# Performance work log

Measured on AMD Instinct MI355X. Metric: run time of the kernel, lower is better.

The kernel has to match this reference:

```python
import jax, jax.numpy as jnp
import numpy as np

GS, GL, LS, LL, NA = 8, 8, 16, 8, 12
ALPHA = 0.5


def _rgb_to_lab(img):
    # img: (B,3,H,W) in [0,1]. Standard sRGB -> CIELab (kornia convention).
    lin = jnp.where(img > 0.04045, ((img + 0.055) / 1.055) ** 2.4, img / 12.92)
    r, g, b = lin[:, 0], lin[:, 1], lin[:, 2]
    x = 0.412453 * r + 0.357580 * g + 0.180423 * b
    y = 0.212671 * r + 0.715160 * g + 0.072169 * b
    z = 0.019334 * r + 0.119193 * g + 0.950227 * b
    xn, yn, zn = x / 0.950456, y, z / 1.088754
    f = lambda t: jnp.where(t > 0.008856, jnp.cbrt(t), 7.787 * t + 4.0 / 29.0)
    fx, fy, fz = f(xn), f(yn), f(zn)
    L = 116.0 * fy - 16.0
    a = 500.0 * (fx - fy)
    bb = 200.0 * (fy - fz)
    return L, a, bb


def _bilateral_slice(grid, img, guide):
    # grid: (B,12,s,s,l); img: (B,3,H,W); guide: (B,H,W) in [0,1]
    B, C, s, _, l = grid.shape
    _, _, H, W = img.shape
    g5 = jnp.transpose(grid, (0, 4, 2, 3, 1))  # (B, D=l, Hg=s, Wg=s, C)
    # align_corners=True coordinates, border padding == clamp
    fx = jnp.linspace(0.0, s - 1.0, W)                    # (W,)
    fy = jnp.linspace(0.0, s - 1.0, H)                    # (H,)
    fz = jnp.clip(guide * (l - 1.0), 0.0, l - 1.0)        # (B,H,W)
    x0 = jnp.floor(fx).astype(jnp.int32); x1 = jnp.minimum(x0 + 1, s - 1)
    y0 = jnp.floor(fy).astype(jnp.int32); y1 = jnp.minimum(y0 + 1, s - 1)
    z0 = jnp.floor(fz).astype(jnp.int32); z1 = jnp.minimum(z0 + 1, l - 1)
    wx = (fx - x0)[None, None, :, None]
    wy = (fy - y0)[None, :, None, None]
    wz = (fz - z0)[..., None]
    bi = jnp.arange(B)[:, None, None]
    yi0, yi1 = y0[None, :, None], y1[None, :, None]
    xi0, xi1 = x0[None, None, :], x1[None, None, :]

    def gat(zi, yi, xi):
        return g5[bi, zi, yi, xi]  # (B,H,W,C)

    def bilin(zi):
        c00 = gat(zi, yi0, xi0) * (1 - wx) + gat(zi, yi0, xi1) * wx
        c10 = gat(zi, yi1, xi0) * (1 - wx) + gat(zi, yi1, xi1) * wx
        return c00 * (1 - wy) + c10 * wy

    coeffs = bilin(z0) * (1 - wz) + bilin(z1) * wz       # (B,H,W,12)
    A = coeffs[..., :9].reshape(B, H, W, 3, 3)
    bvec = coeffs[..., 9:]
    img_hwc = jnp.transpose(img, (0, 2, 3, 1))           # (B,H,W,3)
    out = jnp.einsum('bhwck,bhwk->bhwc', A, img_hwc) + bvec
    return jnp.transpose(jnp.clip(out, 0.0, 1.0), (0, 3, 1, 2))


def setup_inputs() -> dict:
    key = jax.random.key(0)
    ks = jax.random.split(key, 16)
    B, H, W = 4, 896, 896
    n_h = n_w = 64
    inp = {
        'R_spatial': jax.random.normal(ks[0], (B, 256, n_h, n_w), jnp.float32),
        'F_sem': jax.random.normal(ks[1], (B, n_h * n_w, 384), jnp.float32),
        'img': jax.random.uniform(ks[2], (B, 3, H, W), jnp.float32),
        'n_h': n_h,
        'n_w': n_w,
    }
    sc = 0.02
    identity = np.array([1., 0., 0., 0., 1., 0., 0., 0., 1., 0., 0., 0.], np.float32)
    inp['dino_proj_w'] = jax.random.normal(ks[3], (128, 384), jnp.float32) * sc
    inp['dino_proj_b'] = jnp.zeros((128,), jnp.float32)
    inp['fusion_w'] = jax.random.normal(ks[4], (256, 384), jnp.float32) * sc
    inp['fusion_b'] = jnp.zeros((256,), jnp.float32)
    inp['g1_w'] = jax.random.normal(ks[5], (256, 256), jnp.float32) * sc
    inp['g1_b'] = jnp.zeros((256,), jnp.float32)
    inp['g2_w'] = jax.random.normal(ks[6], (NA * GS * GS * GL, 256), jnp.float32) * sc
    inp['g2_b'] = jnp.asarray(np.repeat(identity, GS * GS * GL))  # identity init
    inp['local_w'] = jax.random.normal(ks[7], (NA * LL, 256), jnp.float32) * sc
    inp['local_b'] = jnp.asarray(np.repeat(identity, LL))
    inp['guide_w1'] = jax.random.normal(ks[8], (64, 384), jnp.float32) * sc
    inp['guide_b1'] = jnp.zeros((64,), jnp.float32)
    inp['guide_w2'] = jax.random.normal(ks[9], (1, 64), jnp.float32) * sc
    inp['guide_b2'] = jnp.zeros((1,), jnp.float32)
    return inp


def reference(R_spatial, F_sem, img, n_h, n_w,
              dino_proj_w, dino_proj_b, fusion_w, fusion_b,
              g1_w, g1_b, g2_w, g2_b, local_w, local_b,
              guide_w1, guide_b1, guide_w2, guide_b2):
    B, _, H, W = img.shape
    # ---- GridNet ----
    F_sp = jnp.transpose(F_sem, (0, 2, 1)).reshape(B, 384, n_h, n_w)
    proj = jnp.einsum('bchw,oc->bohw', F_sp, dino_proj_w) + dino_proj_b[None, :, None, None]
    fused_in = jnp.concatenate([R_spatial, proj], axis=1)
    fused = jnp.einsum('bchw,oc->bohw', fused_in, fusion_w) + fusion_b[None, :, None, None]
    f_gap = fused.mean(axis=(-2, -1))                       # (B,256)
    h = jax.nn.relu(f_gap @ g1_w.T + g1_b)
    G_global = (h @ g2_w.T + g2_b).reshape(B, NA, GS, GS, GL)
    kh, kw = n_h // LS, n_w // LS
    pooled = fused.reshape(B, 256, LS, kh, LS, kw).mean(axis=(3, 5))
    lflat = jnp.einsum('bchw,oc->bohw', pooled, local_w) + local_b[None, :, None, None]
    G_local = jnp.transpose(lflat.reshape(B, NA, LL, LS, LS), (0, 1, 3, 4, 2))
    # ---- SemanticGuide ----
    L, a, bb = _rgb_to_lab(img)
    g_chroma = jnp.clip((0.5 * L + 0.25 * jnp.abs(a) + 0.25 * jnp.abs(bb)) / 114.0, 0.0, 1.0)
    hsem = jax.nn.relu(jnp.einsum('bnd,hd->bnh', F_sem, guide_w1) + guide_b1)
    g_sem_patch = jax.nn.sigmoid(jnp.einsum('bnh,oh->bno', hsem, guide_w2) + guide_b2)
    g_sem_patch = g_sem_patch.reshape(B, n_h, n_w, 1).transpose(0, 3, 1, 2)
    g_sem = jax.image.resize(g_sem_patch, (B, 1, H, W), 'bilinear')[:, 0]
    g = ALPHA * g_chroma + (1.0 - ALPHA) * g_sem
    # ---- slice + apply ----
    I_global = _bilateral_slice(G_global, img, g)
    I_local = _bilateral_slice(G_local, img, g)
    return I_global, I_local, G_global, G_local, g
```

## Files before the change

### kernel.cpp

```cpp
#include <hip/hip_runtime.h>
#include <math.h>

#define HWPIX 802816
#define OUT_IL 9633792
#define OUT_GG 19267584
#define OUT_GL 19292160
#define OUT_G  19390464

#define WS_WT4  0
#define WS_BC   163840
#define WS_POOL 164096
#define WS_H    426240
#define WS_GSEM 427264
#define WS_RG   443648
#define WS_RL   468224
#define WS_W1T  566528
#define WS_LWT  591104

__device__ __forceinline__ float fast_exp2(float x) {
  return __builtin_amdgcn_exp2f(x);
}
__device__ __forceinline__ float fast_log2(float x) {
  return __builtin_amdgcn_logf(x);
}
__device__ __forceinline__ float srgb_lin(float v) {
  float p = fast_exp2(2.4f * fast_log2((v + 0.055f) * (1.0f / 1.055f)));
  return v > 0.04045f ? p : v * (1.0f / 12.92f);
}
__device__ __forceinline__ float labf(float t) {
  float c = fast_exp2((1.0f / 3.0f) * fast_log2(t));
  return t > 0.008856f ? c : 7.787f * t + (4.0f / 29.0f);
}

__global__ __launch_bounds__(256) void k_prep(
    const float* __restrict__ fus_w, const float* __restrict__ fus_b,
    const float* __restrict__ dino_w, const float* __restrict__ dino_b,
    const float* __restrict__ gw1, const float* __restrict__ lw,
    float* __restrict__ Wt4, float* __restrict__ bc, float* __restrict__ w1T,
    float* __restrict__ lwT) {
  if (blockIdx.x == 642) {
    int t = threadIdx.x;
    for (int it = 0; it < 96; ++it) {
      int idx = it * 256 + t;
      int o = idx >> 8;
      int c = idx & 255;
      lwT[c * 96 + o] = lw[o * 256 + c];
    }
    return;
  }
  if (blockIdx.x == 641) {
    int t = threadIdx.x;
    for (int it = 0; it < 96; ++it) {
      int idx = it * 256 + t;
      int h = idx & 63;
      int k = idx >> 6;
      w1T[((k >> 2) * 64 + h) * 4 + (k & 3)] = gw1[h * 384 + k];
    }
    return;
  }
  if (blockIdx.x == 640) {
    int o = threadIdx.x;
    float acc = fus_b[o];
    for (int m = 0; m < 128; ++m) acc += fus_w[o * 384 + 256 + m] * dino_b[m];
    bc[o] = acc;
    return;
  }
  int idx = blockIdx.x * 256 + threadIdx.x;
  int o = idx / 640;
  int k = idx - o * 640;
  float val;
  if (k < 256) {
    val = fus_w[o * 384 + k];
  } else {
    int d = k - 256;
    float acc = 0.0f;
    for (int m = 0; m < 128; ++m)
      acc += fus_w[o * 384 + 256 + m] * dino_w[m * 384 + d];
    val = acc;
  }
  Wt4[((k >> 2) * 256 + o) * 4 + (k & 3)] = val;
}

__global__ __launch_bounds__(1024) void k_fused_pool(
    const float* __restrict__ R, const float* __restrict__ F,
    const float* __restrict__ Wt4, const float* __restrict__ bc,
    const float* __restrict__ lwT, const float* __restrict__ lb,
    float* __restrict__ pooled, float* __restrict__ out4,
    float* __restrict__ rl) {
  int blk = blockIdx.x;
  int b = blk >> 6;
  int i = (blk >> 2) & 15;
  int jg = blk & 3;
  int t = threadIdx.x;
  int cell = t >> 8;
  int c = t & 255;
  __shared__ float s[4 * 640];
  {
    const float* rb = R + (((b * 256 + c) * 64 + i * 4) * 64) + (jg * 4 + cell) * 4;
    float p = 0.0f;
#pragma unroll
    for (int di = 0; di < 4; ++di) {
      float4 v = *(const float4*)(rb + di * 64);
      p += v.x + v.y + v.z + v.w;
    }
    s[cell * 640 + c] = p;
  }
  {
    float a0 = 0.0f, a1 = 0.0f;
    const float* fb = F + (size_t)(b * 4096 + (i * 4) * 64 + (jg * 4 + cell) * 4) * 384;
#pragma unroll
    for (int pix = 0; pix < 16; ++pix) {
      const float* fr = fb + (size_t)((pix >> 2) * 64 + (pix & 3)) * 384;
      a0 += fr[c];
      if (c < 128) a1 += fr[256 + c];
    }
    s[cell * 640 + 256 + c] = a0;
    if (c < 128) s[cell * 640 + 512 + c] = a1;
  }
  __syncthreads();
  float acc = 0.0f;
  const float4* w4 = (const float4*)Wt4;
  const float4* s4 = (const float4*)(s + cell * 640);
#pragma unroll 8
  for (int kk = 0; kk < 160; ++kk) {
    float4 wv = w4[kk * 256 + c];
    float4 sv = s4[kk];
    acc += wv.x * sv.x + wv.y * sv.y + wv.z * sv.z + wv.w * sv.w;
  }
  __syncthreads();
  s[cell * 256 + c] = acc;
  __syncthreads();
  if (t < 256) {
    float bco = bc[t];
    float4 v;
    v.x = s[0 * 256 + t] * (1.0f / 16.0f) + bco;
    v.y = s[1 * 256 + t] * (1.0f / 16.0f) + bco;
    v.z = s[2 * 256 + t] * (1.0f / 16.0f) + bco;
    v.w = s[3 * 256 + t] * (1.0f / 16.0f) + bco;
    *(float4*)(pooled + ((size_t)(b * 256 + t) * 256) + i * 16 + jg * 4) = v;
  } else if (t < 640) {
    int idx = t - 256;
    int cl = idx / 96;
    int o = idx - cl * 96;
    const float* sc_ = s + cl * 256;
    float acc2 = lb[o];
    for (int cc = 0; cc < 256; ++cc) {
      float pv = sc_[cc] * (1.0f / 16.0f) + bc[cc];
      acc2 += lwT[cc * 96 + o] * pv;
    }
    int cellg = i * 16 + jg * 4 + cl;
    int n = o >> 3, l = o & 7;
    out4[((b * 12 + n) * 256 + cellg) * 8 + l] = acc2;
    rl[b * 24576 + (cellg * 8 + l) * 12 + n] = acc2;
  }
}

__global__ __launch_bounds__(1024) void k_gap(
    const float* __restrict__ pooled, const float* __restrict__ g1_w,
    const float* __restrict__ g1_b, float* __restrict__ hout) {
  int b = blockIdx.x;
  int t = threadIdx.x;
  int o = t & 255;
  int q = t >> 8;
  __shared__ float f[256];
  __shared__ float part[4][256];
  {
    const float4* pr4 = (const float4*)(pooled + (size_t)(b * 256 + o) * 256 + q * 64);
    float s = 0.0f;
#pragma unroll
    for (int i = 0; i < 16; ++i) {
      float4 v = pr4[i];
      s += v.x + v.y + v.z + v.w;
    }
    part[q][o] = s;
  }
  __syncthreads();
  if (t < 256)
    f[t] = (part[0][t] + part[1][t] + part[2][t] + part[3][t]) * (1.0f / 256.0f);
  __syncthreads();
  {
    const float4* wr = (const float4*)(g1_w + o * 256 + q * 64);
    const float4* fq = (const float4*)(f + q * 64);
    float acc = 0.0f;
#pragma unroll
    for (int i = 0; i < 16; ++i) {
      float4 w = wr[i];
      float4 fv = fq[i];
      acc += w.x * fv.x + w.y * fv.y + w.z * fv.z + w.w * fv.w;
    }
    part[q][o] = acc;
  }
  __syncthreads();
  if (t < 256) {
    float a = part[0][t] + part[1][t] + part[2][t] + part[3][t] + g1_b[t];
    hout[b * 256 + t] = fmaxf(a, 0.0f);
  }
}

__global__ __launch_bounds__(1024) void k_gglobal(
    const float* __restrict__ h, const float* __restrict__ g2_w,
    const float* __restrict__ g2_b, float* __restrict__ out3,
    float* __restrict__ rg) {
  int b = blockIdx.x / 24;
  int og = (blockIdx.x % 24) * 256;
  int t = threadIdx.x;
  int ol = t & 255;
  int q = t >> 8;
  __shared__ float hl[256];
  __shared__ float part[4][256];
  if (t < 256) hl[t] = h[b * 256 + t];
  __syncthreads();
  {
    const float4* wr = (const float4*)(g2_w + (size_t)(og + ol) * 256 + q * 64);
    const float4* hq = (const float4*)(hl + q * 64);
    float acc = 0.0f;
#pragma unroll
    for (int i = 0; i < 16; ++i) {
      float4 w = wr[i];
      float4 hv = hq[i];
      acc += w.x * hv.x + w.y * hv.y + w.z * hv.z + w.w * hv.w;
    }
    part[q][ol] = acc;
  }
  __syncthreads();
  if (t < 256) {
    int o = og + t;
    float a = part[0][t] + part[1][t] + part[2][t] + part[3][t] + g2_b[o];
    out3[b * 6144 + o] = a;
    int n = o >> 9, y = (o >> 6) & 7, x = (o >> 3) & 7, z = o & 7;
    rg[b * 6144 + ((y * 8 + x) * 8 + z) * 12 + n] = a;
  }
}

__global__ __launch_bounds__(256) void k_guide(
    const float* __restrict__ F, const float* __restrict__ w1T,
    const float* __restrict__ b1, const float* __restrict__ w2,
    const float* __restrict__ b2, float* __restrict__ gsem) {
  int t = threadIdx.x;
  int wave = t >> 6;
  int lane = t & 63;
  int pb = blockIdx.x * 16;
  __shared__ float4 sF[16 * 96];
  const float4* Fb = (const float4*)(F + (size_t)pb * 384);
#pragma unroll
  for (int r = 0; r < 6; ++r) sF[r * 256 + t] = Fb[r * 256 + t];
  __syncthreads();
  float accp[4] = {0.0f, 0.0f, 0.0f, 0.0f};
  const float4* w4 = (const float4*)w1T;
  int prow = wave * 4;
  for (int c = 0; c < 48; ++c) {
    float4 wa = w4[(c * 2 + 0) * 64 + lane];
    float4 wb = w4[(c * 2 + 1) * 64 + lane];
#pragma unroll
    for (int p = 0; p < 4; ++p) {
      float4 va = sF[(prow + p) * 96 + c * 2 + 0];
      float4 vb = sF[(prow + p) * 96 + c * 2 + 1];
      accp[p] += va.x * wa.x + va.y * wa.y + va.z * wa.z + va.w * wa.w +
                 vb.x * wb.x + vb.y * wb.y + vb.z * wb.z + vb.w * wb.w;
    }
  }
  float hb = b1[lane];
  float wl = w2[lane];
  float b2v = b2[0];
  float res = 0.0f;
#pragma unroll
  for (int p = 0; p < 4; ++p) {
    float v = fmaxf(accp[p] + hb, 0.0f) * wl;
#pragma unroll
    for (int m = 32; m >= 1; m >>= 1) v += __shfl_xor(v, m, 64);
    if (lane == p) res = v;
  }
  if (lane < 4) gsem[pb + prow + lane] = 1.0f / (1.0f + expf(-(res + b2v)));
}

template <int SDIM>
__device__ __forceinline__ void slice_lds(
    const float* __restrict__ sg, int w, int z0, int z1, float wz,
    float r, float g, float bl, float& o0, float& o1, float& o2) {
  constexpr float sc = (float)(SDIM - 1) * (1.0f / 895.0f);
  float fxs = (float)w * sc;
  int x0 = (int)fxs;
  if (x0 > SDIM - 1) x0 = SDIM - 1;
  int x1 = x0 < SDIM - 1 ? x0 + 1 : SDIM - 1;
  float wx = fxs - (float)x0;
  float wz0 = 1.0f - wz;
  float w00 = (1.0f - wx) * wz0;
  float w01 = (1.0f - wx) * wz;
  float w10 = wx * wz0;
  float w11 = wx * wz;
  const float4* p00 = (const float4*)(sg + (x0 * 8 + z0) * 12);
  const float4* p01 = (const float4*)(sg + (x0 * 8 + z1) * 12);
  const float4* p10 = (const float4*)(sg + (x1 * 8 + z0) * 12);
  const float4* p11 = (const float4*)(sg + (x1 * 8 + z1) * 12);
  float a[12];
#pragma unroll
  for (int c = 0; c < 3; ++c) {
    float4 v00 = p00[c], v01 = p01[c], v10 = p10[c], v11 = p11[c];
    a[4 * c + 0] = w00 * v00.x + w01 * v01.x + w10 * v10.x + w11 * v11.x;
    a[4 * c + 1] = w00 * v00.y + w01 * v01.y + w10 * v10.y + w11 * v11.y;
    a[4 * c + 2] = w00 * v00.z + w01 * v01.z + w10 * v10.z + w11 * v11.z;
    a[4 * c + 3] = w00 * v00.w + w01 * v01.w + w10 * v10.w + w11 * v11.w;
  }
  o0 = fminf(fmaxf(a[0] * r + a[1] * g + a[2] * bl + a[9], 0.0f), 1.0f);
  o1 = fminf(fmaxf(a[3] * r + a[4] * g + a[5] * bl + a[10], 0.0f), 1.0f);
  o2 = fminf(fmaxf(a[6] * r + a[7] * g + a[8] * bl + a[11], 0.0f), 1.0f);
}

__global__ __launch_bounds__(448) void k_pixel(
    const float* __restrict__ img, const float* __restrict__ gsem,
    const float* __restrict__ rg, const float* __restrict__ rl,
    float* __restrict__ out) {
  int blk = blockIdx.x;
  int b = blk / 896;
  int h = blk - b * 896;
  int t = threadIdx.x;
  __shared__ float sgr[64];
  __shared__ float sG[768];
  __shared__ float sL[1536];

  float sy = fminf(fmaxf((h + 0.5f) * (1.0f / 14.0f) - 0.5f, 0.0f), 63.0f);
  int y0s = (int)sy;
  int y1s = y0s < 63 ? y0s + 1 : 63;
  float wys = sy - (float)y0s;
  float fyg = (float)h * (7.0f / 895.0f);
  int y0g = (int)fyg;
  if (y0g > 7) y0g = 7;
  int y1g = y0g < 7 ? y0g + 1 : 7;
  float wyg = fyg - (float)y0g;
  float fyl = (float)h * (15.0f / 895.0f);
  int y0l = (int)fyl;
  if (y0l > 15) y0l = 15;
  int y1l = y0l < 15 ? y0l + 1 : 15;
  float wyl = fyl - (float)y0l;

  if (t < 64) {
    const float* gb = gsem + b * 4096;
    sgr[t] = gb[y0s * 64 + t] * (1.0f - wys) + gb[y1s * 64 + t] * wys;
  }
  {
    const float* g0 = rg + b * 6144 + y0g * 768;
    const float* g1 = rg + b * 6144 + y1g * 768;
    for (int i = t; i < 768; i += 448)
      sG[i] = g0[i] * (1.0f - wyg) + g1[i] * wyg;
    const float* l0 = rl + b * 24576 + y0l * 1536;
    const float* l1 = rl + b * 24576 + y1l * 1536;
    for (int i = t; i < 1536; i += 448)
      sL[i] = l0[i] * (1.0f - wyl) + l1[i] * wyl;
  }
  __syncthreads();

#pragma unroll
  for (int ip = 0; ip < 2; ++ip) {
    int w = ip * 448 + t;
    int hw = h * 896 + w;
    float r = img[(b * 3 + 0) * HWPIX + hw];
    float g = img[(b * 3 + 1) * HWPIX + hw];
    float bl = img[(b * 3 + 2) * HWPIX + hw];
    float lr = srgb_lin(r), lg = srgb_lin(g), lb2 = srgb_lin(bl);
    float X = 0.412453f * lr + 0.357580f * lg + 0.180423f * lb2;
    float Y = 0.212671f * lr + 0.715160f * lg + 0.072169f * lb2;
    float Z = 0.019334f * lr + 0.119193f * lg + 0.950227f * lb2;
    float fx_ = labf(X * (1.0f / 0.950456f));
    float fy_ = labf(Y);
    float fz_ = labf(Z * (1.0f / 1.088754f));
    float gch = 0.50877193f * fy_ - 0.070175439f +
                1.0964912f * fabsf(fx_ - fy_) + 0.43859649f * fabsf(fy_ - fz_);
    gch = fminf(fmaxf(gch, 0.0f), 1.0f);
    float sx = fminf(fmaxf((w + 0.5f) * (1.0f / 14.0f) - 0.5f, 0.0f), 63.0f);
    int x0s = (int)sx;
    int x1s = x0s < 63 ? x0s + 1 : 63;
    float wxs = sx - (float)x0s;
    float gs = sgr[x0s] * (1.0f - wxs) + sgr[x1s] * wxs;
    float gg = 0.5f * gch + 0.5f * gs;
    __builtin_nontemporal_store(gg, &out[OUT_G + b * HWPIX + hw]);
    float fzc = fminf(fmaxf(gg * 7.0f, 0.0f), 7.0f);
    int z0 = (int)fzc;
    if (z0 > 7) z0 = 7;
    int z1 = z0 < 7 ? z0 + 1 : 7;
    float wz = fzc - (float)z0;
    float o0, o1, o2;
    slice_lds<8>(sG, w, z0, z1, wz, r, g, bl, o0, o1, o2);
    __builtin_nontemporal_store(o0, &out[(b * 3 + 0) * HWPIX + hw]);
    __builtin_nontemporal_store(o1, &out[(b * 3 + 1) * HWPIX + hw]);
    __builtin_nontemporal_store(o2, &out[(b * 3 + 2) * HWPIX + hw]);
    slice_lds<16>(sL, w, z0, z1, wz, r, g, bl, o0, o1, o2);
    __builtin_nontemporal_store(o0, &out[OUT_IL + (b * 3 + 0) * HWPIX + hw]);
    __builtin_nontemporal_store(o1, &out[OUT_IL + (b * 3 + 1) * HWPIX + hw]);
    __builtin_nontemporal_store(o2, &out[OUT_IL + (b * 3 + 2) * HWPIX + hw]);
  }
}

extern "C" void kernel_launch(void* const* d_in, const int* in_sizes, int n_in,
                              void* d_out, int out_size, void* d_ws,
                              size_t ws_size, hipStream_t stream) {
  const float* R = (const float*)d_in[0];
  const float* F = (const float*)d_in[1];
  const float* img = (const float*)d_in[2];
  const float* dino_w = (const float*)d_in[5];
  const float* dino_b = (const float*)d_in[6];
  const float* fus_w = (const float*)d_in[7];
  const float* fus_b = (const float*)d_in[8];
  const float* g1_w = (const float*)d_in[9];
  const float* g1_b = (const float*)d_in[10];
  const float* g2_w = (const float*)d_in[11];
  const float* g2_b = (const float*)d_in[12];
  const float* lw = (const float*)d_in[13];
  const float* lb = (const float*)d_in[14];
  const float* gw1 = (const float*)d_in[15];
  const float* gb1 = (const float*)d_in[16];
  const float* gw2 = (const float*)d_in[17];
  const float* gb2 = (const float*)d_in[18];
  float* out = (float*)d_out;
  float* ws = (float*)d_ws;

  float* Wt4 = ws + WS_WT4;
  float* bc = ws + WS_BC;
  float* pooled = ws + WS_POOL;
  float* hbuf = ws + WS_H;
  float* gsem = ws + WS_GSEM;
  float* rg = ws + WS_RG;
  float* rl = ws + WS_RL;
  float* w1T = ws + WS_W1T;
  float* lwT = ws + WS_LWT;

  k_prep<<<643, 256, 0, stream>>>(fus_w, fus_b, dino_w, dino_b, gw1, lw,
                                  Wt4, bc, w1T, lwT);
  k_guide<<<1024, 256, 0, stream>>>(F, w1T, gb1, gw2, gb2, gsem);
  k_fused_pool<<<256, 1024, 0, stream>>>(R, F, Wt4, bc, lwT, lb,
                                         pooled, out + OUT_GL, rl);
  k_gap<<<4, 1024, 0, stream>>>(pooled, g1_w, g1_b, hbuf);
  k_gglobal<<<96, 1024, 0, stream>>>(hbuf, g2_w, g2_b, out + OUT_GG, rg);
  k_pixel<<<3584, 448, 0, stream>>>(img, gsem, rg, rl, out);
}
```

Baseline: 318.1 us.

## Fuse GAP and global head kernels, retile guide MLP, prefetch pixel loads

Merges k_gap and k_gglobal into one k_head kernel. Each of its 96 blocks recomputes the pooled mean and first layer instead of round-tripping through a workspace buffer, which saves one launch at the cost of redundant work. k_guide changes its w1T layout and lane mapping so each lane handles a quarter of K for four hidden groups, with a padded LDS layout and shuffle reductions. k_pixel issues its image and grid-row loads up front, before the LDS staging, so their latency overlaps the setup.

```diff
diff --git a/kernel.cpp b/kernel.cpp
--- a/kernel.cpp
+++ b/kernel.cpp
@@ -54,7 +54,12 @@
       int idx = it * 256 + t;
       int h = idx & 63;
       int k = idx >> 6;
-      w1T[((k >> 2) * 64 + h) * 4 + (k & 3)] = gw1[h * 384 + k];
+      int kq = k / 96;
+      int krem = k - kq * 96;
+      int k4 = krem >> 2;
+      int j = krem & 3;
+      int hg = h >> 4, hl = h & 15;
+      w1T[((((kq * 24 + k4) * 4 + hg) * 16) + hl) * 4 + j] = gw1[h * 384 + k];
     }
     return;
   }
@@ -155,50 +160,9 @@
   }
 }
 
-__global__ __launch_bounds__(1024) void k_gap(
+__global__ __launch_bounds__(1024) void k_head(
     const float* __restrict__ pooled, const float* __restrict__ g1_w,
-    const float* __restrict__ g1_b, float* __restrict__ hout) {
-  int b = blockIdx.x;
-  int t = threadIdx.x;
-  int o = t & 255;
-  int q = t >> 8;
-  __shared__ float f[256];
-  __shared__ float part[4][256];
-  {
-    const float4* pr4 = (const float4*)(pooled + (size_t)(b * 256 + o) * 256 + q * 64);
-    float s = 0.0f;
-#pragma unroll
-    for (int i = 0; i < 16; ++i) {
-      float4 v = pr4[i];
-      s += v.x + v.y + v.z + v.w;
-    }
-    part[q][o] = s;
-  }
-  __syncthreads();
-  if (t < 256)
-    f[t] = (part[0][t] + part[1][t] + part[2][t] + part[3][t]) * (1.0f / 256.0f);
-  __syncthreads();
-  {
-    const float4* wr = (const float4*)(g1_w + o * 256 + q * 64);
-    const float4* fq = (const float4*)(f + q * 64);
-    float acc = 0.0f;
-#pragma unroll
-    for (int i = 0; i < 16; ++i) {
-      float4 w = wr[i];
-      float4 fv = fq[i];
-      acc += w.x * fv.x + w.y * fv.y + w.z * fv.z + w.w * fv.w;
-    }
-    part[q][o] = acc;
-  }
-  __syncthreads();
-  if (t < 256) {
-    float a = part[0][t] + part[1][t] + part[2][t] + part[3][t] + g1_b[t];
-    hout[b * 256 + t] = fmaxf(a, 0.0f);
-  }
-}
-
-__global__ __launch_bounds__(1024) void k_gglobal(
-    const float* __restrict__ h, const float* __restrict__ g2_w,
+    const float* __restrict__ g1_b, const float* __restrict__ g2_w,
     const float* __restrict__ g2_b, float* __restrict__ out3,
     float* __restrict__ rg) {
   int b = blockIdx.x / 24;
@@ -206,19 +170,48 @@
   int t = threadIdx.x;
   int ol = t & 255;
   int q = t >> 8;
-  __shared__ float hl[256];
   __shared__ float part[4][256];
-  if (t < 256) hl[t] = h[b * 256 + t];
+  __shared__ float f[256];
+  __shared__ float hv[256];
+  {
+    const float4* pr4 = (const float4*)(pooled + (size_t)(b * 256 + ol) * 256 + q * 64);
+    float s = 0.0f;
+#pragma unroll
+    for (int i = 0; i < 16; ++i) {
+      float4 v = pr4[i];
+      s += v.x + v.y + v.z + v.w;
+    }
+    part[q][ol] = s;
+  }
+  __syncthreads();
+  if (t < 256)
+    f[t] = (part[0][t] + part[1][t] + part[2][t] + part[3][t]) * (1.0f / 256.0f);
+  __syncthreads();
+  {
+    const float4* wr = (const float4*)(g1_w + (size_t)ol * 256 + q * 64);
+    const float4* fq = (const float4*)(f + q * 64);
+    float acc = 0.0f;
+#pragma unroll
+    for (int i = 0; i < 16; ++i) {
+      float4 w = wr[i];
+      float4 v = fq[i];
+      acc += w.x * v.x + w.y * v.y + w.z * v.z + w.w * v.w;
+    }
+    part[q][ol] = acc;
+  }
+  __syncthreads();
+  if (t < 256)
+    hv[t] = fmaxf(part[0][t] + part[1][t] + part[2][t] + part[3][t] + g1_b[t], 0.0f);
   __syncthreads();
   {
     const float4* wr = (const float4*)(g2_w + (size_t)(og + ol) * 256 + q * 64);
-    const float4* hq = (const float4*)(hl + q * 64);
+    const float4* hq = (const float4*)(hv + q * 64);
     float acc = 0.0f;
 #pragma unroll
     for (int i = 0; i < 16; ++i) {
       float4 w = wr[i];
-      float4 hv = hq[i];
-      acc += w.x * hv.x + w.y * hv.y + w.z * hv.z + w.w * hv.w;
+      float4 v = hq[i];
+      acc += w.x * v.x + w.y * v.y + w.z * v.z + w.w * v.w;
     }
     part[q][ol] = acc;
   }
@@ -239,35 +232,67 @@
   int t = threadIdx.x;
   int wave = t >> 6;
   int lane = t & 63;
+  int kq = lane >> 4;
+  int hl = lane & 15;
   int pb = blockIdx.x * 16;
-  __shared__ float4 sF[16 * 96];
+  __shared__ float4 sF[16 * 4 * 25];
   const float4* Fb = (const float4*)(F + (size_t)pb * 384);
 #pragma unroll
-  for (int r = 0; r < 6; ++r) sF[r * 256 + t] = Fb[r * 256 + t];
-  __syncthreads();
-  float accp[4] = {0.0f, 0.0f, 0.0f, 0.0f};
+  for (int r6 = 0; r6 < 6; ++r6) {
+    int g = r6 * 256 + t;
+    int row = g / 96;
+    int col = g - row * 96;
+    int cq = col / 24;
+    int c4 = col - cq * 24;
+    sF[(row * 4 + cq) * 25 + c4] = Fb[g];
+  }
+  __syncthreads();
+  float acc[4][4];
+#pragma unroll
+  for (int p = 0; p < 4; ++p)
+#pragma unroll
+    for (int hg = 0; hg < 4; ++hg) acc[p][hg] = 0.0f;
   const float4* w4 = (const float4*)w1T;
   int prow = wave * 4;
-  for (int c = 0; c < 48; ++c) {
-    float4 wa = w4[(c * 2 + 0) * 64 + lane];
-    float4 wb = w4[(c * 2 + 1) * 64 + lane];
+  for (int k4 = 0; k4 < 24; ++k4) {
+    float4 wv0 = w4[((kq * 24 + k4) * 4 + 0) * 16 + hl];
+    float4 wv1 = w4[((kq * 24 + k4) * 4 + 1) * 16 + hl];
+    float4 wv2 = w4[((kq * 24 + k4) * 4 + 2) * 16 + hl];
+    float4 wv3 = w4[((kq * 24 + k4) * 4 + 3) * 16 + hl];
 #pragma unroll
     for (int p = 0; p < 4; ++p) {
-      float4 va = sF[(prow + p) * 96 + c * 2 + 0];
-      float4 vb = sF[(prow + p) * 96 + c * 2 + 1];
-      accp[p] += va.x * wa.x + va.y * wa.y + va.z * wa.z + va.w * wa.w +
-                 vb.x * wb.x + vb.y * wb.y + vb.z * wb.z + vb.w * wb.w;
-    }
-  }
-  float hb = b1[lane];
-  float wl = w2[lane];
+      float4 fv = sF[((prow + p) * 4 + kq) * 25 + k4];
+      acc[p][0] += fv.x * wv0.x + fv.y * wv0.y + fv.z * wv0.z + fv.w * wv0.w;
+      acc[p][1] += fv.x * wv1.x + fv.y * wv1.y + fv.z * wv1.z + fv.w * wv1.w;
+      acc[p][2] += fv.x * wv2.x + fv.y * wv2.y + fv.z * wv2.z + fv.w * wv2.w;
+      acc[p][3] += fv.x * wv3.x + fv.y * wv3.y + fv.z * wv3.z + fv.w * wv3.w;
+    }
+  }
+#pragma unroll
+  for (int p = 0; p < 4; ++p)
+#pragma unroll
+    for (int hg = 0; hg < 4; ++hg) {
+      float v = acc[p][hg];
+      v += __shfl_xor(v, 16, 64);
+      v += __shfl_xor(v, 32, 64);
+      acc[p][hg] = v;
+    }
+  float b1v[4], w2v[4];
+#pragma unroll
+  for (int hg = 0; hg < 4; ++hg) {
+    b1v[hg] = b1[hg * 16 + hl];
+    w2v[hg] = w2[hg * 16 + hl];
+  }
   float b2v = b2[0];
   float res = 0.0f;
 #pragma unroll
   for (int p = 0; p < 4; ++p) {
-    float v = fmaxf(accp[p] + hb, 0.0f) * wl;
-#pragma unroll
-    for (int m = 32; m >= 1; m >>= 1) v += __shfl_xor(v, m, 64);
+    float v = 0.0f;
+#pragma unroll
+    for (int hg = 0; hg < 4; ++hg)
+      v += fmaxf(acc[p][hg] + b1v[hg], 0.0f) * w2v[hg];
+#pragma unroll
+    for (int m = 8; m >= 1; m >>= 1) v += __shfl_xor(v, m, 64);
     if (lane == p) res = v;
   }
   if (lane < 4) gsem[pb + prow + lane] = 1.0f / (1.0f + expf(-(res + b2v)));
@@ -318,6 +343,13 @@
   __shared__ float sG[768];
   __shared__ float sL[1536];
 
+  int hwA = h * 896 + t;
+  int hwB = hwA + 448;
+  const float* imb = img + (size_t)b * 3 * HWPIX;
+  float rrA = imb[hwA],             rrB = imb[hwB];
+  float ggA = imb[HWPIX + hwA],     ggB = imb[HWPIX + hwB];
+  float bbA = imb[2 * HWPIX + hwA], bbB = imb[2 * HWPIX + hwB];
+
   float sy = fminf(fmaxf((h + 0.5f) * (1.0f / 14.0f) - 0.5f, 0.0f), 63.0f);
   int y0s = (int)sy;
   int y1s = y0s < 63 ? y0s + 1 : 63;
@@ -333,29 +365,41 @@
   int y1l = y0l < 15 ? y0l + 1 : 15;
   float wyl = fyl - (float)y0l;
 
+  const float* g0 = rg + b * 6144 + y0g * 768;
+  const float* g1 = rg + b * 6144 + y1g * 768;
+  const float* l0 = rl + b * 24576 + y0l * 1536;
+  const float* l1 = rl + b * 24576 + y1l * 1536;
+  float ga0 = g0[t], gb0 = g1[t];
+  float ga1 = 0.0f, gb1 = 0.0f;
+  if (t < 320) { ga1 = g0[t + 448]; gb1 = g1[t + 448]; }
+  float la0 = l0[t], lb0 = l1[t];
+  float la1 = l0[t + 448], lb1 = l1[t + 448];
+  float la2 = l0[t + 896], lb2s = l1[t + 896];
+  float la3 = 0.0f, lb3 = 0.0f;
+  if (t < 192) { la3 = l0[t + 1344]; lb3 = l1[t + 1344]; }
+  float sg0 = 0.0f, sg1 = 0.0f;
   if (t < 64) {
-    const float* gb = gsem + b * 4096;
-    sgr[t] = gb[y0s * 64 + t] * (1.0f - wys) + gb[y1s * 64 + t] * wys;
-  }
-  {
-    const float* g0 = rg + b * 6144 + y0g * 768;
-    const float* g1 = rg + b * 6144 + y1g * 768;
-    for (int i = t; i < 768; i += 448)
-      sG[i] = g0[i] * (1.0f - wyg) + g1[i] * wyg;
-    const float* l0 = rl + b * 24576 + y0l * 1536;
-    const float* l1 = rl + b * 24576 + y1l * 1536;
-    for (int i = t; i < 1536; i += 448)
-      sL[i] = l0[i] * (1.0f - wyl) + l1[i] * wyl;
-  }
-  __syncthreads();
-
+    const float* gbp = gsem + b * 4096;
+    sg0 = gbp[y0s * 64 + t];
+    sg1 = gbp[y1s * 64 + t];
+  }
+  sG[t] = ga0 * (1.0f - wyg) + gb0 * wyg;
+  if (t < 320) sG[t + 448] = ga1 * (1.0f - wyg) + gb1 * wyg;
+  sL[t] = la0 * (1.0f - wyl) + lb0 * wyl;
+  sL[t + 448] = la1 * (1.0f - wyl) + lb1 * wyl;
+  sL[t + 896] = la2 * (1.0f - wyl) + lb2s * wyl;
+  if (t < 192) sL[t + 1344] = la3 * (1.0f - wyl) + lb3 * wyl;
+  if (t < 64) sgr[t] = sg0 * (1.0f - wys) + sg1 * wys;
+  __syncthreads();
+
+  float rr_[2] = {rrA, rrB}, gg_[2] = {ggA, ggB}, bb_[2] = {bbA, bbB};
 #pragma unroll
   for (int ip = 0; ip < 2; ++ip) {
     int w = ip * 448 + t;
     int hw = h * 896 + w;
-    float r = img[(b * 3 + 0) * HWPIX + hw];
-    float g = img[(b * 3 + 1) * HWPIX + hw];
-    float bl = img[(b * 3 + 2) * HWPIX + hw];
+    float r = rr_[ip];
+    float g = gg_[ip];
+    float bl = bb_[ip];
     float lr = srgb_lin(r), lg = srgb_lin(g), lb2 = srgb_lin(bl);
     float X = 0.412453f * lr + 0.357580f * lg + 0.180423f * lb2;
     float Y = 0.212671f * lr + 0.715160f * lg + 0.072169f * lb2;
@@ -416,7 +460,6 @@
   float* Wt4 = ws + WS_WT4;
   float* bc = ws + WS_BC;
   float* pooled = ws + WS_POOL;
-  float* hbuf = ws + WS_H;
   float* gsem = ws + WS_GSEM;
   float* rg = ws + WS_RG;
   float* rl = ws + WS_RL;
@@ -428,7 +471,7 @@
   k_guide<<<1024, 256, 0, stream>>>(F, w1T, gb1, gw2, gb2, gsem);
   k_fused_pool<<<256, 1024, 0, stream>>>(R, F, Wt4, bc, lwT, lb,
                                          pooled, out + OUT_GL, rl);
-  k_gap<<<4, 1024, 0, stream>>>(pooled, g1_w, g1_b, hbuf);
-  k_gglobal<<<96, 1024, 0, stream>>>(hbuf, g2_w, g2_b, out + OUT_GG, rg);
+  k_head<<<96, 1024, 0, stream>>>(pooled, g1_w, g1_b, g2_w, g2_b,
+                                  out + OUT_GG, rg);
   k_pixel<<<3584, 448, 0, stream>>>(img, gsem, rg, rl, out);
 }
```

Result: faster. 306.8 us (-3.6%).
